# Performance work log

Measured on AMD Instinct MI355X. Metric: run time of the kernel, lower is better.

Reference implementation:

```python
import jax, jax.numpy as jnp
import numpy as np


def setup_inputs() -> dict:
    key = jax.random.key(0)
    k1, k2, k3 = jax.random.split(key, 3)
    B, T, F, U = 32, 4096, 512, 512
    x = jax.random.normal(k1, (B, T, F), dtype=jnp.float32)
    W = jax.random.normal(k2, (F, U), dtype=jnp.float32)
    b = jnp.zeros((U,), dtype=jnp.float32)
    V = jax.random.uniform(k3, (U, 1), dtype=jnp.float32)
    return {"x": x, "W": W, "b": b, "V": V}


def reference(x, W, b, V):
    # u = tanh(x @ W + b): [B, T, U]
    u = jnp.tanh(jnp.einsum('btf,fu->btu', x, W) + b)
    # scores = u @ V: [B, T, 1]; softmax over time (dim=1)
    a = jax.nn.softmax(jnp.einsum('btu,uo->bto', u, V), axis=1)
    # weighted sum pooling over time -> [B, F]
    return jnp.sum(x * a, axis=1)
```

## Files before the change

kernel.cpp:

```cpp
#include <hip/hip_runtime.h>


#define XB 32
#define XT 4096
#define XF 512
#define XU 512
#define ROWS (XB * XT)

typedef __attribute__((ext_vector_type(8))) short short8;
typedef __attribute__((ext_vector_type(4))) float f32x4;

__device__ inline void cvt_hilo(float x, unsigned short &h, unsigned short &l) {
  unsigned u = __builtin_bit_cast(unsigned, x);
  h = (unsigned short)(u >> 16);
  float hf = __builtin_bit_cast(float, u & 0xFFFF0000u);
  float lo = x - hf;
  l = (unsigned short)(__builtin_bit_cast(unsigned, lo) >> 16);
}

__device__ inline void async_ld16(const void *g, void *l) {
  __builtin_amdgcn_global_load_lds(
      (const __attribute__((address_space(1))) unsigned int *)g,
      (__attribute__((address_space(3))) unsigned int *)l, 16, 0, 0);
}

__device__ inline float tanh_fast(float z) {
  float e = __expf(2.0f * z);
  return 1.0f - 2.0f * __builtin_amdgcn_rcpf(e + 1.0f);
}

__global__ void wconv_kernel(const float *__restrict__ W,
                             unsigned short *__restrict__ whi,
                             unsigned short *__restrict__ wlo) {
  int t = blockIdx.x * 256 + threadIdx.x;
  int n = t & 511;
  int kg = (t >> 9) & 3;
  int kw = t >> 11;
  int kbase = kw * 32 + kg * 8;
  short8 hv, lv;
#pragma unroll
  for (int j = 0; j < 8; ++j) {
    unsigned short h, l;
    cvt_hilo(W[(size_t)(kbase + j) * XU + n], h, l);
    hv[j] = (short)h;
    lv[j] = (short)l;
  }
  size_t off = (size_t)kw * 16384 + (size_t)n * 32 + (size_t)kg * 8;
  *(short8 *)(whi + off) = hv;
  *(short8 *)(wlo + off) = lv;
}

__global__ __launch_bounds__(256, 2)
void gemm_scores_kernel(const float *__restrict__ x,
                        const unsigned short *__restrict__ whi,
                        const unsigned short *__restrict__ wlo,
                        const float *__restrict__ bias,
                        const float *__restrict__ V,
                        float *__restrict__ scores) {
  __shared__ unsigned short wsm[32768];

  const int tid = threadIdx.x;
  const int lane = tid & 63;
  const int wave = tid >> 6;
  const int wr = wave >> 1;
  const int wc = wave & 1;
  const int quad = lane >> 4;
  const int l15 = lane & 15;
  const size_t rowbase = (size_t)blockIdx.x * 64;

  f32x4 acc[2][16];
#pragma unroll
  for (int a = 0; a < 2; ++a)
#pragma unroll
    for (int c = 0; c < 16; ++c) acc[a][c] = (f32x4){0.f, 0.f, 0.f, 0.f};

  const float *xr0 = x + (rowbase + (size_t)wr * 32 + l15) * XF + quad * 8;
  const float *xr1 = xr0 + 16 * XF;
  const int cg0 = wave * 16;

#pragma unroll 1
  for (int kw = 0; kw < 16; ++kw) {
#pragma unroll
    for (int i = 0; i < 16; ++i) {
      int cg = cg0 + i;
      int var = cg >> 5;
      int c = cg & 31;
      const unsigned short *g =
          (var ? wlo : whi) + (size_t)kw * 16384 + c * 512 + lane * 8;
      unsigned short *lp = wsm + var * 16384 + c * 512 + lane * 8;
      async_ld16(g, lp);
    }
    const float *p0 = xr0 + kw * 32;
    const float *p1 = xr1 + kw * 32;
    float4 a00 = *(const float4 *)(p0);
    float4 a01 = *(const float4 *)(p0 + 4);
    float4 a10 = *(const float4 *)(p1);
    float4 a11 = *(const float4 *)(p1 + 4);

    __syncthreads();

    short8 ah0, al0, ah1, al1;
    {
      float v0[8] = {a00.x, a00.y, a00.z, a00.w, a01.x, a01.y, a01.z, a01.w};
      float v1[8] = {a10.x, a10.y, a10.z, a10.w, a11.x, a11.y, a11.z, a11.w};
#pragma unroll
      for (int j = 0; j < 8; ++j) {
        unsigned short h, l;
        cvt_hilo(v0[j], h, l);
        ah0[j] = (short)h; al0[j] = (short)l;
        cvt_hilo(v1[j], h, l);
        ah1[j] = (short)h; al1[j] = (short)l;
      }
    }

#pragma unroll
    for (int cf = 0; cf < 16; ++cf) {
      const unsigned short *bp =
          wsm + ((wc * 256 + cf * 16 + l15) * 4 + quad) * 8;
      short8 bh = *(const short8 *)bp;
      short8 bl = *(const short8 *)(bp + 16384);
      acc[0][cf] = __builtin_amdgcn_mfma_f32_16x16x32_bf16(ah0, bh, acc[0][cf], 0, 0, 0);
      acc[1][cf] = __builtin_amdgcn_mfma_f32_16x16x32_bf16(ah1, bh, acc[1][cf], 0, 0, 0);
      acc[0][cf] = __builtin_amdgcn_mfma_f32_16x16x32_bf16(al0, bh, acc[0][cf], 0, 0, 0);
      acc[1][cf] = __builtin_amdgcn_mfma_f32_16x16x32_bf16(al1, bh, acc[1][cf], 0, 0, 0);
      acc[0][cf] = __builtin_amdgcn_mfma_f32_16x16x32_bf16(ah0, bl, acc[0][cf], 0, 0, 0);
      acc[1][cf] = __builtin_amdgcn_mfma_f32_16x16x32_bf16(ah1, bl, acc[1][cf], 0, 0, 0);
    }
    __syncthreads();
  }

  float sc0[4] = {0.f, 0.f, 0.f, 0.f};
  float sc1[4] = {0.f, 0.f, 0.f, 0.f};
#pragma unroll
  for (int cf = 0; cf < 16; ++cf) {
    int n = wc * 256 + cf * 16 + l15;
    float vv = V[n];
    float bb = bias[n];
#pragma unroll
    for (int r = 0; r < 4; ++r) {
      sc0[r] += tanh_fast(acc[0][cf][r] + bb) * vv;
      sc1[r] += tanh_fast(acc[1][cf][r] + bb) * vv;
    }
  }
#pragma unroll
  for (int m = 1; m <= 8; m <<= 1) {
#pragma unroll
    for (int r = 0; r < 4; ++r) {
      sc0[r] += __shfl_xor(sc0[r], m, 64);
      sc1[r] += __shfl_xor(sc1[r], m, 64);
    }
  }
  float *scb = (float *)wsm;
  if (l15 == 0) {
    int base = wc * 64 + wr * 32 + quad * 4;
#pragma unroll
    for (int r = 0; r < 4; ++r) {
      scb[base + r] = sc0[r];
      scb[base + 16 + r] = sc1[r];
    }
  }
  __syncthreads();
  if (tid < 64) scores[rowbase + tid] = scb[tid] + scb[64 + tid];
}

__global__ void stats_kernel(const float *__restrict__ scores,
                             float *__restrict__ stats) {
  int b = blockIdx.x, tid = threadIdx.x;
  const float *s = scores + (size_t)b * XT;
  float v[16];
#pragma unroll
  for (int i = 0; i < 16; ++i) v[i] = s[tid + i * 256];
  float mx = v[0];
#pragma unroll
  for (int i = 1; i < 16; ++i) mx = fmaxf(mx, v[i]);
  for (int m = 1; m < 64; m <<= 1) mx = fmaxf(mx, __shfl_xor(mx, m, 64));
  __shared__ float redm[4], reds[4];
  if ((tid & 63) == 0) redm[tid >> 6] = mx;
  __syncthreads();
  mx = fmaxf(fmaxf(redm[0], redm[1]), fmaxf(redm[2], redm[3]));
  float sum = 0.f;
#pragma unroll
  for (int i = 0; i < 16; ++i) sum += __expf(v[i] - mx);
  for (int m = 1; m < 64; m <<= 1) sum += __shfl_xor(sum, m, 64);
  if ((tid & 63) == 0) reds[tid >> 6] = sum;
  __syncthreads();
  if (tid == 0) {
    stats[b * 2] = mx;
    stats[b * 2 + 1] = reds[0] + reds[1] + reds[2] + reds[3];
  }
}

__global__ __launch_bounds__(256)
void pool_kernel(const float *__restrict__ x, const float *__restrict__ scores,
                 const float *__restrict__ stats, float *__restrict__ out) {
  int b = blockIdx.x >> 4;
  int ch = blockIdx.x & 15;
  int tid = threadIdx.x;
  __shared__ float w[256];
  float mx = stats[b * 2];
  float inv = 1.0f / stats[b * 2 + 1];
  int t0 = ch * 256;
  w[tid] = __expf(scores[(size_t)b * XT + t0 + tid] - mx) * inv;
  __syncthreads();
  const float *xp = x + ((size_t)b * XT + t0) * XF;
  float a0 = 0.f, a1 = 0.f;
#pragma unroll 4
  for (int t = 0; t < 256; ++t) {
    float wv = w[t];
    a0 += wv * xp[(size_t)t * XF + tid];
    a1 += wv * xp[(size_t)t * XF + tid + 256];
  }
  atomicAdd(&out[b * XF + tid], a0);
  atomicAdd(&out[b * XF + tid + 256], a1);
}

extern "C" void kernel_launch(void *const *d_in, const int *in_sizes, int n_in,
                              void *d_out, int out_size, void *d_ws,
                              size_t ws_size, hipStream_t stream) {
  const float *x = (const float *)d_in[0];
  const float *W = (const float *)d_in[1];
  const float *bias = (const float *)d_in[2];
  const float *V = (const float *)d_in[3];
  float *out = (float *)d_out;

  unsigned short *whi = (unsigned short *)d_ws;
  unsigned short *wlo = whi + 262144;
  float *scores = (float *)((char *)d_ws + 1048576);
  float *stats = (float *)((char *)d_ws + 1572864);

  hipMemsetAsync(d_out, 0, (size_t)out_size * sizeof(float), stream);
  wconv_kernel<<<128, 256, 0, stream>>>(W, whi, wlo);
  gemm_scores_kernel<<<2048, 256, 0, stream>>>(x, whi, wlo, bias, V, scores);
  stats_kernel<<<32, 256, 0, stream>>>(scores, stats);
  pool_kernel<<<512, 256, 0, stream>>>(x, scores, stats, out);
}
```

Before: 575.2 us.

## Switch GEMM to 32x32 MFMA with direct-from-global W fragments and vectorize pooling

The scores GEMM now uses 512-thread blocks covering 128 rows, with 32x32x16 bf16 MFMAs in place of 16x16x32. It drops the LDS staging of W and its block barriers: each wave loads its hi/lo W fragments straight from global memory (L2-resident) in a layout that wconv_kernel writes to match. The pool kernel is restructured to read float4 rows, use 128-timestep chunks with two row-groups reduced through LDS, and launch twice as many blocks. The aim is fewer barriers and fewer MFMA issues per FLOP, but W traffic from L2 rises and register pressure is higher.

```diff
diff --git a/kernel.cpp b/kernel.cpp
--- a/kernel.cpp
+++ b/kernel.cpp
@@ -1,14 +1,13 @@
 #include <hip/hip_runtime.h>
 
 
-#define XB 32
 #define XT 4096
 #define XF 512
 #define XU 512
-#define ROWS (XB * XT)
+#define ROWS (32 * 4096)
 
 typedef __attribute__((ext_vector_type(8))) short short8;
-typedef __attribute__((ext_vector_type(4))) float f32x4;
+typedef __attribute__((ext_vector_type(16))) float f32x16;
 
 __device__ inline void cvt_hilo(float x, unsigned short &h, unsigned short &l) {
   unsigned u = __builtin_bit_cast(unsigned, x);
@@ -18,12 +17,6 @@
   l = (unsigned short)(__builtin_bit_cast(unsigned, lo) >> 16);
 }
 
-__device__ inline void async_ld16(const void *g, void *l) {
-  __builtin_amdgcn_global_load_lds(
-      (const __attribute__((address_space(1))) unsigned int *)g,
-      (__attribute__((address_space(3))) unsigned int *)l, 16, 0, 0);
-}
-
 __device__ inline float tanh_fast(float z) {
   float e = __expf(2.0f * z);
   return 1.0f - 2.0f * __builtin_amdgcn_rcpf(e + 1.0f);
@@ -32,72 +25,69 @@
 __global__ void wconv_kernel(const float *__restrict__ W,
                              unsigned short *__restrict__ whi,
                              unsigned short *__restrict__ wlo) {
-  int t = blockIdx.x * 256 + threadIdx.x;
-  int n = t & 511;
-  int kg = (t >> 9) & 3;
-  int kw = t >> 11;
-  int kbase = kw * 32 + kg * 8;
+  int t2 = blockIdx.x * 256 + threadIdx.x;
+  int l = t2 & 31;
+  int g = (t2 >> 5) & 1;
+  int t = (t2 >> 6) & 15;
+  int s = t2 >> 10;
   short8 hv, lv;
 #pragma unroll
   for (int j = 0; j < 8; ++j) {
-    unsigned short h, l;
-    cvt_hilo(W[(size_t)(kbase + j) * XU + n], h, l);
+    unsigned short h, lo;
+    cvt_hilo(W[(size_t)(s * 16 + g * 8 + j) * XU + t * 32 + l], h, lo);
     hv[j] = (short)h;
-    lv[j] = (short)l;
-  }
-  size_t off = (size_t)kw * 16384 + (size_t)n * 32 + (size_t)kg * 8;
+    lv[j] = (short)lo;
+  }
+  size_t off = (size_t)s * 8192 + t * 512 + g * 256 + l * 8;
   *(short8 *)(whi + off) = hv;
   *(short8 *)(wlo + off) = lv;
 }
 
-__global__ __launch_bounds__(256, 2)
+__global__ __launch_bounds__(512, 2)
 void gemm_scores_kernel(const float *__restrict__ x,
                         const unsigned short *__restrict__ whi,
                         const unsigned short *__restrict__ wlo,
                         const float *__restrict__ bias,
                         const float *__restrict__ V,
                         float *__restrict__ scores) {
-  __shared__ unsigned short wsm[32768];
+  __shared__ float scb[512];
 
   const int tid = threadIdx.x;
   const int lane = tid & 63;
   const int wave = tid >> 6;
-  const int wr = wave >> 1;
-  const int wc = wave & 1;
-  const int quad = lane >> 4;
-  const int l15 = lane & 15;
-  const size_t rowbase = (size_t)blockIdx.x * 64;
-
-  f32x4 acc[2][16];
+  const int wr = wave >> 2;
+  const int wc = wave & 3;
+  const int l31 = lane & 31;
+  const int half = lane >> 5;
+  const size_t rowbase = (size_t)blockIdx.x * 128;
+
+  f32x16 acc[2][4];
 #pragma unroll
   for (int a = 0; a < 2; ++a)
 #pragma unroll
-    for (int c = 0; c < 16; ++c) acc[a][c] = (f32x4){0.f, 0.f, 0.f, 0.f};
-
-  const float *xr0 = x + (rowbase + (size_t)wr * 32 + l15) * XF + quad * 8;
-  const float *xr1 = xr0 + 16 * XF;
-  const int cg0 = wave * 16;
+    for (int c = 0; c < 4; ++c)
+#pragma unroll
+      for (int r = 0; r < 16; ++r) acc[a][c][r] = 0.f;
+
+  const float *xr0 = x + (rowbase + wr * 64 + l31) * XF + half * 8;
+  const float *xr1 = xr0 + 32 * XF;
+  const unsigned short *whp = whi + (size_t)(wc * 4) * 512 + lane * 8;
+  const unsigned short *wlp = wlo + (size_t)(wc * 4) * 512 + lane * 8;
 
 #pragma unroll 1
-  for (int kw = 0; kw < 16; ++kw) {
-#pragma unroll
-    for (int i = 0; i < 16; ++i) {
-      int cg = cg0 + i;
-      int var = cg >> 5;
-      int c = cg & 31;
-      const unsigned short *g =
-          (var ? wlo : whi) + (size_t)kw * 16384 + c * 512 + lane * 8;
-      unsigned short *lp = wsm + var * 16384 + c * 512 + lane * 8;
-      async_ld16(g, lp);
+  for (int s = 0; s < 32; ++s) {
+    short8 bh[4], bl[4];
+    const unsigned short *p = whp + (size_t)s * 8192;
+    const unsigned short *q = wlp + (size_t)s * 8192;
+#pragma unroll
+    for (int cf = 0; cf < 4; ++cf) {
+      bh[cf] = *(const short8 *)(p + cf * 512);
+      bl[cf] = *(const short8 *)(q + cf * 512);
     }
-    const float *p0 = xr0 + kw * 32;
-    const float *p1 = xr1 + kw * 32;
-    float4 a00 = *(const float4 *)(p0);
-    float4 a01 = *(const float4 *)(p0 + 4);
-    float4 a10 = *(const float4 *)(p1);
-    float4 a11 = *(const float4 *)(p1 + 4);
-
-    __syncthreads();
+    float4 a00 = *(const float4 *)(xr0 + s * 16);
+    float4 a01 = *(const float4 *)(xr0 + s * 16 + 4);
+    float4 a10 = *(const float4 *)(xr1 + s * 16);
+    float4 a11 = *(const float4 *)(xr1 + s * 16 + 4);
 
     short8 ah0, al0, ah1, al1;
     {
@@ -105,62 +95,63 @@
       float v1[8] = {a10.x, a10.y, a10.z, a10.w, a11.x, a11.y, a11.z, a11.w};
 #pragma unroll
       for (int j = 0; j < 8; ++j) {
-        unsigned short h, l;
-        cvt_hilo(v0[j], h, l);
-        ah0[j] = (short)h; al0[j] = (short)l;
-        cvt_hilo(v1[j], h, l);
-        ah1[j] = (short)h; al1[j] = (short)l;
+        unsigned short h, lo;
+        cvt_hilo(v0[j], h, lo);
+        ah0[j] = (short)h; al0[j] = (short)lo;
+        cvt_hilo(v1[j], h, lo);
+        ah1[j] = (short)h; al1[j] = (short)lo;
       }
     }
 
 #pragma unroll
-    for (int cf = 0; cf < 16; ++cf) {
-      const unsigned short *bp =
-          wsm + ((wc * 256 + cf * 16 + l15) * 4 + quad) * 8;
-      short8 bh = *(const short8 *)bp;
-      short8 bl = *(const short8 *)(bp + 16384);
-      acc[0][cf] = __builtin_amdgcn_mfma_f32_16x16x32_bf16(ah0, bh, acc[0][cf], 0, 0, 0);
-      acc[1][cf] = __builtin_amdgcn_mfma_f32_16x16x32_bf16(ah1, bh, acc[1][cf], 0, 0, 0);
-      acc[0][cf] = __builtin_amdgcn_mfma_f32_16x16x32_bf16(al0, bh, acc[0][cf], 0, 0, 0);
-      acc[1][cf] = __builtin_amdgcn_mfma_f32_16x16x32_bf16(al1, bh, acc[1][cf], 0, 0, 0);
-      acc[0][cf] = __builtin_amdgcn_mfma_f32_16x16x32_bf16(ah0, bl, acc[0][cf], 0, 0, 0);
-      acc[1][cf] = __builtin_amdgcn_mfma_f32_16x16x32_bf16(ah1, bl, acc[1][cf], 0, 0, 0);
+    for (int cf = 0; cf < 4; ++cf) {
+      acc[0][cf] = __builtin_amdgcn_mfma_f32_32x32x16_bf16(ah0, bh[cf], acc[0][cf], 0, 0, 0);
+      acc[1][cf] = __builtin_amdgcn_mfma_f32_32x32x16_bf16(ah1, bh[cf], acc[1][cf], 0, 0, 0);
+      acc[0][cf] = __builtin_amdgcn_mfma_f32_32x32x16_bf16(al0, bh[cf], acc[0][cf], 0, 0, 0);
+      acc[1][cf] = __builtin_amdgcn_mfma_f32_32x32x16_bf16(al1, bh[cf], acc[1][cf], 0, 0, 0);
+      acc[0][cf] = __builtin_amdgcn_mfma_f32_32x32x16_bf16(ah0, bl[cf], acc[0][cf], 0, 0, 0);
+      acc[1][cf] = __builtin_amdgcn_mfma_f32_32x32x16_bf16(ah1, bl[cf], acc[1][cf], 0, 0, 0);
     }
-    __syncthreads();
-  }
-
-  float sc0[4] = {0.f, 0.f, 0.f, 0.f};
-  float sc1[4] = {0.f, 0.f, 0.f, 0.f};
-#pragma unroll
-  for (int cf = 0; cf < 16; ++cf) {
-    int n = wc * 256 + cf * 16 + l15;
+  }
+
+  float sc[2][16];
+#pragma unroll
+  for (int rf = 0; rf < 2; ++rf)
+#pragma unroll
+    for (int r = 0; r < 16; ++r) sc[rf][r] = 0.f;
+
+#pragma unroll
+  for (int cf = 0; cf < 4; ++cf) {
+    int n = wc * 128 + cf * 32 + l31;
     float vv = V[n];
     float bb = bias[n];
 #pragma unroll
-    for (int r = 0; r < 4; ++r) {
-      sc0[r] += tanh_fast(acc[0][cf][r] + bb) * vv;
-      sc1[r] += tanh_fast(acc[1][cf][r] + bb) * vv;
-    }
-  }
-#pragma unroll
-  for (int m = 1; m <= 8; m <<= 1) {
-#pragma unroll
-    for (int r = 0; r < 4; ++r) {
-      sc0[r] += __shfl_xor(sc0[r], m, 64);
-      sc1[r] += __shfl_xor(sc1[r], m, 64);
-    }
-  }
-  float *scb = (float *)wsm;
-  if (l15 == 0) {
-    int base = wc * 64 + wr * 32 + quad * 4;
-#pragma unroll
-    for (int r = 0; r < 4; ++r) {
-      scb[base + r] = sc0[r];
-      scb[base + 16 + r] = sc1[r];
-    }
-  }
-  __syncthreads();
-  if (tid < 64) scores[rowbase + tid] = scb[tid] + scb[64 + tid];
+    for (int rf = 0; rf < 2; ++rf)
+#pragma unroll
+      for (int r = 0; r < 16; ++r)
+        sc[rf][r] += tanh_fast(acc[rf][cf][r] + bb) * vv;
+  }
+#pragma unroll
+  for (int m = 1; m <= 16; m <<= 1) {
+#pragma unroll
+    for (int rf = 0; rf < 2; ++rf)
+#pragma unroll
+      for (int r = 0; r < 16; ++r)
+        sc[rf][r] += __shfl_xor(sc[rf][r], m, 64);
+  }
+  if (l31 == 0) {
+#pragma unroll
+    for (int rf = 0; rf < 2; ++rf)
+#pragma unroll
+      for (int r = 0; r < 16; ++r) {
+        int row = wr * 64 + rf * 32 + (r & 3) + 8 * (r >> 2) + 4 * half;
+        scb[wc * 128 + row] = sc[rf][r];
+      }
+  }
+  __syncthreads();
+  if (tid < 128)
+    scores[rowbase + tid] =
+        scb[tid] + scb[128 + tid] + scb[256 + tid] + scb[384 + tid];
 }
 
 __global__ void stats_kernel(const float *__restrict__ scores,
@@ -193,25 +184,43 @@
 __global__ __launch_bounds__(256)
 void pool_kernel(const float *__restrict__ x, const float *__restrict__ scores,
                  const float *__restrict__ stats, float *__restrict__ out) {
-  int b = blockIdx.x >> 4;
-  int ch = blockIdx.x & 15;
+  int b = blockIdx.x >> 5;
+  int ch = blockIdx.x & 31;
   int tid = threadIdx.x;
-  __shared__ float w[256];
+  __shared__ float w[128];
+  __shared__ float red[512];
   float mx = stats[b * 2];
   float inv = 1.0f / stats[b * 2 + 1];
-  int t0 = ch * 256;
-  w[tid] = __expf(scores[(size_t)b * XT + t0 + tid] - mx) * inv;
-  __syncthreads();
-  const float *xp = x + ((size_t)b * XT + t0) * XF;
-  float a0 = 0.f, a1 = 0.f;
+  if (tid < 128)
+    w[tid] = __expf(scores[(size_t)b * XT + ch * 128 + tid] - mx) * inv;
+  __syncthreads();
+  int c = tid & 127;
+  int ro = tid >> 7;
+  const float *xp = x + ((size_t)b * XT + ch * 128) * XF;
+  float4 a = {0.f, 0.f, 0.f, 0.f};
 #pragma unroll 4
-  for (int t = 0; t < 256; ++t) {
-    float wv = w[t];
-    a0 += wv * xp[(size_t)t * XF + tid];
-    a1 += wv * xp[(size_t)t * XF + tid + 256];
-  }
-  atomicAdd(&out[b * XF + tid], a0);
-  atomicAdd(&out[b * XF + tid + 256], a1);
+  for (int i = 0; i < 64; ++i) {
+    int r = i * 2 + ro;
+    float4 v = *(const float4 *)(xp + (size_t)r * XF + c * 4);
+    float wv = w[r];
+    a.x += wv * v.x;
+    a.y += wv * v.y;
+    a.z += wv * v.z;
+    a.w += wv * v.w;
+  }
+  if (ro == 1) {
+    red[c * 4 + 0] = a.x;
+    red[c * 4 + 1] = a.y;
+    red[c * 4 + 2] = a.z;
+    red[c * 4 + 3] = a.w;
+  }
+  __syncthreads();
+  if (ro == 0) {
+    atomicAdd(&out[b * XF + c * 4 + 0], a.x + red[c * 4 + 0]);
+    atomicAdd(&out[b * XF + c * 4 + 1], a.y + red[c * 4 + 1]);
+    atomicAdd(&out[b * XF + c * 4 + 2], a.z + red[c * 4 + 2]);
+    atomicAdd(&out[b * XF + c * 4 + 3], a.w + red[c * 4 + 3]);
+  }
 }
 
 extern "C" void kernel_launch(void *const *d_in, const int *in_sizes, int n_in,
@@ -230,7 +239,7 @@
 
   hipMemsetAsync(d_out, 0, (size_t)out_size * sizeof(float), stream);
   wconv_kernel<<<128, 256, 0, stream>>>(W, whi, wlo);
-  gemm_scores_kernel<<<2048, 256, 0, stream>>>(x, whi, wlo, bias, V, scores);
+  gemm_scores_kernel<<<1024, 512, 0, stream>>>(x, whi, wlo, bias, V, scores);
   stats_kernel<<<32, 256, 0, stream>>>(scores, stats);
-  pool_kernel<<<512, 256, 0, stream>>>(x, scores, stats, out);
-}
+  pool_kernel<<<1024, 256, 0, stream>>>(x, scores, stats, out);
+}
```

After: 572.9 us. Within noise of the previous version (-0.4%).
